# Performance work log

Hardware: AMD Instinct MI355X
Metric: run time of the kernel (lower is better)

## Reference

```python
import jax, jax.numpy as jnp
import numpy as np

N, D, K = 65536, 128, 1024
DECAY = 0.99
COMMITMENT_COST = 0.25
TEMPERATURE = 1.0
TAU = 1.0


def setup_inputs() -> dict:
    key = jax.random.key(0)
    k1, k2 = jax.random.split(key)
    return {
        "inputs": jax.random.normal(k1, (N, D), dtype=jnp.float32),
        "codebook": jax.random.normal(k2, (K, D), dtype=jnp.float32),
    }


def reference(inputs, codebook):
    # Flatten to (N, D) token view (already flat here).
    x = inputs.reshape(-1, codebook.shape[1])

    # torch.cdist(x, codebook, p=2): Euclidean pairwise distances, shape (N, K).
    d2 = (
        jnp.sum(x * x, axis=1, keepdims=True)
        + jnp.sum(codebook * codebook, axis=1)[None, :]
        - 2.0 * (x @ codebook.T)
    )
    dist = jnp.sqrt(jnp.maximum(d2, 1e-12))

    # F.gumbel_softmax(-dist / temperature, tau=1.0, hard=True)
    logits = -dist / TEMPERATURE
    gumbels = jax.random.gumbel(jax.random.key(42), logits.shape, logits.dtype)
    y_soft = jax.nn.softmax((logits + gumbels) / TAU, axis=-1)
    idx = jnp.argmax(y_soft, axis=-1)
    y_hard = jax.nn.one_hot(idx, codebook.shape[0], dtype=logits.dtype)
    # Straight-through estimator: hard forward, soft backward.
    codes = y_hard + y_soft - jax.lax.stop_gradient(y_soft)  # (N, K)

    quantized = codes @ codebook  # (N, D)
    quantization_loss = jnp.mean((quantized - x) ** 2)
    commitment_loss = COMMITMENT_COST * jnp.mean(
        (x - jax.lax.stop_gradient(codes) @ jax.lax.stop_gradient(codebook)) ** 2
    )
    loss = quantization_loss + commitment_loss

    # In-place .data EMA codebook update: scatter-accumulate via one-hot transpose matmul.
    new_codebook = DECAY * codebook + (1.0 - DECAY) * (
        jax.lax.stop_gradient(codes).T @ jax.lax.stop_gradient(x)
    )

    return codes, loss, new_codebook
```

## Files before the change

### kernel.cpp

```cpp
#include <hip/hip_runtime.h>
#include <stdint.h>
#include <math.h>

#define NTOK 65536
#define DIM  128
#define KC   1024
#define MARGIN 1e-2f

static __device__ __forceinline__ uint32_t tf_xor(uint32_t j) {
  const uint32_t K0 = 0u, K1 = 42u, K2 = 0x1BD11BDAu ^ K0 ^ K1;
  const uint32_t ks[3] = {K0, K1, K2};
  uint32_t x0 = K0;
  uint32_t x1 = j + K1;
#pragma unroll
  for (int i = 0; i < 5; ++i) {
    const int rA[4] = {13, 15, 26, 6};
    const int rB[4] = {17, 29, 16, 24};
#pragma unroll
    for (int r4 = 0; r4 < 4; ++r4) {
      const int r = (i & 1) ? rB[r4] : rA[r4];
      x0 += x1;
      x1 = (x1 << r) | (x1 >> (32 - r));
      x1 ^= x0;
    }
    x0 += ks[(i + 1) % 3];
    x1 += ks[(i + 2) % 3] + (uint32_t)(i + 1);
  }
  return x0 ^ x1;
}

static __device__ __forceinline__ float gumbf(uint32_t b) {
  const float tiny = 1.17549435e-38f;
  float f = __uint_as_float((b >> 9) | 0x3f800000u) - 1.0f;
  float u = (f > 0.0f) ? f : tiny;
  return -__logf(-__logf(u)) * 1.0f + 0.0f;
}

static __device__ __forceinline__ float gumb32(uint32_t b) {
  double f = (double)(b >> 9) * (1.0 / 8388608.0);
  const double tiny = 1.1754943508222875e-38;
  double u = (f > 0.0) ? f : tiny;
  return (float)(-log(-log(u)));
}

__global__ void vq_cnorm(const float* __restrict__ cb, double* __restrict__ cnorm,
                         float* __restrict__ lpart, uint32_t* __restrict__ fix_count) {
  const int k = blockIdx.x;
  const int t = threadIdx.x;
  double a = (double)cb[k * DIM + t];
  double b = (double)cb[k * DIM + 64 + t];
  double s = a * a + b * b;
#pragma unroll
  for (int off = 32; off >= 1; off >>= 1) s += __shfl_down(s, off, 64);
  if (t == 0) { cnorm[k] = s; lpart[k] = 0.0f; }
  if (k == 0 && t == 0) fix_count[0] = 0u;
}

__global__ __launch_bounds__(256, 2)
void vq_main(const float* __restrict__ x, const float* __restrict__ cb,
             const double* __restrict__ cnorm, uint32_t* __restrict__ out_idx,
             uint32_t* __restrict__ fix_count, uint32_t* __restrict__ fix_list) {
  __shared__ float xs[64 * 132];
  __shared__ float cs[64 * 132];
  __shared__ float xn_s[64];
  __shared__ float cn_s[64];

  const int tid = threadIdx.x;
  const int blk = blockIdx.x;
  const int rg = tid >> 4;
  const int cg = tid & 15;

  {
    const float4* xg = (const float4*)x;
#pragma unroll
    for (int q = 0; q < 8; ++q) {
      int li = tid + q * 256;
      int row = li >> 5, c4 = li & 31;
      *(float4*)(xs + row * 132 + c4 * 4) = xg[blk * 2048 + li];
    }
  }
  __syncthreads();
  if (tid < 64) {
    float s = 0.0f;
    const float* p = xs + tid * 132;
#pragma unroll
    for (int d = 0; d < DIM; ++d) s = fmaf(p[d], p[d], s);
    xn_s[tid] = s;
  }
  __syncthreads();

  const int r0 = 4 * rg;
  float xn[4] = {xn_s[r0], xn_s[r0 + 1], xn_s[r0 + 2], xn_s[r0 + 3]};
  const uint32_t R0g = (uint32_t)(blk * 64 + r0);
  const uint32_t jb[4] = {(R0g + 0u) << 10, (R0g + 1u) << 10,
                          (R0g + 2u) << 10, (R0g + 3u) << 10};

  float b1[4] = {-1e30f, -1e30f, -1e30f, -1e30f};
  float b2[4] = {-1e30f, -1e30f, -1e30f, -1e30f};
  int   k1[4] = {0, 0, 0, 0};

  const float* xp[4] = {xs + r0 * 132, xs + (r0 + 1) * 132,
                        xs + (r0 + 2) * 132, xs + (r0 + 3) * 132};
  const float* cp[4] = {cs + (cg + 0) * 132, cs + (cg + 16) * 132,
                        cs + (cg + 32) * 132, cs + (cg + 48) * 132};

  for (int kt = 0; kt < 16; ++kt) {
    {
      const float4* cg4 = (const float4*)cb;
#pragma unroll
      for (int q = 0; q < 8; ++q) {
        int li = tid + q * 256;
        int row = li >> 5, c4 = li & 31;
        *(float4*)(cs + row * 132 + c4 * 4) = cg4[kt * 2048 + li];
      }
      if (tid < 64) cn_s[tid] = (float)cnorm[kt * 64 + tid];
    }
    __syncthreads();

    float acc[4][4];
#pragma unroll
    for (int i = 0; i < 4; ++i)
#pragma unroll
      for (int j = 0; j < 4; ++j) acc[i][j] = 0.0f;

#pragma unroll 4
    for (int d = 0; d < DIM; d += 4) {
      float4 xv[4], cv[4];
#pragma unroll
      for (int i = 0; i < 4; ++i) xv[i] = *(const float4*)(xp[i] + d);
#pragma unroll
      for (int j = 0; j < 4; ++j) cv[j] = *(const float4*)(cp[j] + d);
#pragma unroll
      for (int i = 0; i < 4; ++i)
#pragma unroll
        for (int j = 0; j < 4; ++j) {
          acc[i][j] = fmaf(xv[i].x, cv[j].x, acc[i][j]);
          acc[i][j] = fmaf(xv[i].y, cv[j].y, acc[i][j]);
          acc[i][j] = fmaf(xv[i].z, cv[j].z, acc[i][j]);
          acc[i][j] = fmaf(xv[i].w, cv[j].w, acc[i][j]);
        }
    }

#pragma unroll
    for (int j = 0; j < 4; ++j) {
      const int kj = cg + 16 * j;
      const int kg = (kt << 6) + kj;
      const float cn = cn_s[kj];
#pragma unroll
      for (int i = 0; i < 4; ++i) {
        const uint32_t fj = jb[i] + (uint32_t)kg;
        const float tiny = 1.17549435e-38f;
        uint32_t bts = tf_xor(fj);
        float f = __uint_as_float((bts >> 9) | 0x3f800000u) - 1.0f;
        float u = (f > 0.0f) ? f : tiny;
        float g = -logf(-logf(u));
        float d2 = (xn[i] + cn) - 2.0f * acc[i][j];
        float dist = sqrtf(fmaxf(d2, 1e-12f));
        float z = g - dist;
        if (z > b1[i]) { b2[i] = b1[i]; b1[i] = z; k1[i] = kg; }
        else if (z > b2[i]) b2[i] = z;
      }
    }
    __syncthreads();
  }

#pragma unroll
  for (int off = 8; off >= 1; off >>= 1) {
#pragma unroll
    for (int i = 0; i < 4; ++i) {
      float ov1 = __shfl_down(b1[i], off, 16);
      int   ok1 = __shfl_down(k1[i], off, 16);
      float ov2 = __shfl_down(b2[i], off, 16);
      if (ov1 > b1[i] || (ov1 == b1[i] && ok1 < k1[i])) {
        b2[i] = fmaxf(b1[i], ov2);
        b1[i] = ov1; k1[i] = ok1;
      } else {
        b2[i] = fmaxf(b2[i], ov1);
      }
    }
  }
  if (cg == 0) {
#pragma unroll
    for (int i = 0; i < 4; ++i) {
      out_idx[R0g + i] = (uint32_t)k1[i];
      if (b1[i] - b2[i] < MARGIN) {
        uint32_t pos = atomicAdd(fix_count, 1u);
        if (pos < NTOK) fix_list[pos] = R0g + i;
      }
    }
  }
}

__global__ __launch_bounds__(256)
void vq_fixup(const float* __restrict__ x, const float* __restrict__ cb,
              const double* __restrict__ cnorm, const uint32_t* __restrict__ fix_count,
              const uint32_t* __restrict__ fix_list, uint32_t* __restrict__ out_idx) {
  __shared__ float xrow[DIM];
  __shared__ double xn_sh;
  __shared__ double bz_sh[256];
  __shared__ int    bk_sh[256];

  const int t = threadIdx.x;
  const uint32_t cnt = fix_count[0];

  for (uint32_t e = blockIdx.x; e < cnt && e < NTOK; e += gridDim.x) {
    const uint32_t row = fix_list[e];
    if (t < 32) ((float4*)xrow)[t] = ((const float4*)(x + (size_t)row * DIM))[t];
    __syncthreads();
    if (t == 0) {
      double s = 0.0;
#pragma unroll
      for (int d = 0; d < DIM; ++d) s = fma((double)xrow[d], (double)xrow[d], s);
      xn_sh = s;
    }
    __syncthreads();
    const double xn = xn_sh;
    const uint32_t jb = row << 10;

    double bz = -1e300;
    int bk = 0;
#pragma unroll
    for (int q = 0; q < 4; ++q) {
      const int kg = t + q * 256;
      float acc = 0.0f;
      const float* crow = cb + (size_t)kg * DIM;
#pragma unroll
      for (int d = 0; d < DIM; ++d) acc = fmaf(xrow[d], crow[d], acc);
      float g = gumb32(tf_xor(jb + (uint32_t)kg));
      double d2 = (xn + cnorm[kg]) - 2.0 * (double)acc;
      double dist = sqrt(fmax(d2, 1e-12));
      double z = (double)g - dist;
      if (z > bz) { bz = z; bk = kg; }
    }
    bz_sh[t] = bz; bk_sh[t] = bk;
    __syncthreads();
    for (int s = 128; s >= 1; s >>= 1) {
      if (t < s) {
        double ov = bz_sh[t + s]; int ok = bk_sh[t + s];
        if (ov > bz_sh[t] || (ov == bz_sh[t] && ok < bk_sh[t])) {
          bz_sh[t] = ov; bk_sh[t] = ok;
        }
      }
      __syncthreads();
    }
    if (t == 0) out_idx[row] = (uint32_t)bk_sh[0];
    __syncthreads();
  }
}

__global__ void vq_ema_init(const float* __restrict__ cb, float* __restrict__ ncb) {
  int i = blockIdx.x * blockDim.x + threadIdx.x;
  ncb[i] = 0.99f * cb[i];
}

__global__ __launch_bounds__(128)
void vq_finish(const float* __restrict__ x, const float* __restrict__ cb,
               const uint32_t* __restrict__ idx, float* __restrict__ codes,
               float* __restrict__ ncb, float* __restrict__ lpart) {
  const int i = blockIdx.x;
  const int t = threadIdx.x;
  const int k = (int)idx[i];

  float xv = x[i * DIM + t];
  float cv = cb[k * DIM + t];
  float d = cv - xv;
  float s = d * d;
#pragma unroll
  for (int off = 32; off >= 1; off >>= 1) s += __shfl_down(s, off, 64);
  __shared__ float sw[2];
  if ((t & 63) == 0) sw[t >> 6] = s;

  atomicAdd(ncb + k * DIM + t, 0.01f * xv);

  float4* crow = (float4*)(codes + (size_t)i * KC);
#pragma unroll
  for (int q = 0; q < 2; ++q) {
    int base = q * 512 + t * 4;
    float4 v = make_float4(0.f, 0.f, 0.f, 0.f);
    int dlt = k - base;
    if (dlt >= 0 && dlt < 4) ((float*)&v)[dlt] = 1.0f;
    crow[base >> 2] = v;
  }

  __syncthreads();
  if (t == 0) atomicAdd(lpart + (i & 1023), sw[0] + sw[1]);
}

__global__ void vq_loss_final(const float* __restrict__ lpart, float* __restrict__ loss) {
  const int t = threadIdx.x;
  float s = 0.0f;
#pragma unroll
  for (int q = 0; q < 4; ++q) s += lpart[t + q * 256];
#pragma unroll
  for (int off = 32; off >= 1; off >>= 1) s += __shfl_down(s, off, 64);
  __shared__ float sw[4];
  if ((t & 63) == 0) sw[t >> 6] = s;
  __syncthreads();
  if (t == 0) {
    float total = (sw[0] + sw[1]) + (sw[2] + sw[3]);
    loss[0] = 1.25f * (total / 8388608.0f);
  }
}

extern "C" void kernel_launch(void* const* d_in, const int* in_sizes, int n_in,
                              void* d_out, int out_size, void* d_ws, size_t ws_size,
                              hipStream_t stream) {
  const float* x  = (const float*)d_in[0];
  const float* cb = (const float*)d_in[1];

  float* codes = (float*)d_out;
  float* loss  = (float*)d_out + (size_t)NTOK * KC;
  float* ncb   = loss + 1;

  uint32_t* idx       = (uint32_t*)d_ws;
  double*   cnorm     = (double*)(idx + NTOK);
  float*    lpart     = (float*)(cnorm + KC);
  uint32_t* fix_count = (uint32_t*)(lpart + KC);
  uint32_t* fix_list  = fix_count + 64;

  vq_cnorm<<<KC, 64, 0, stream>>>(cb, cnorm, lpart, fix_count);
  vq_main<<<1024, 256, 0, stream>>>(x, cb, cnorm, idx, fix_count, fix_list);
  vq_fixup<<<256, 256, 0, stream>>>(x, cb, cnorm, fix_count, fix_list, idx);
  vq_ema_init<<<512, 256, 0, stream>>>(cb, ncb);
  vq_finish<<<NTOK, 128, 0, stream>>>(x, cb, idx, codes, ncb, lpart);
  vq_loss_final<<<1, 256, 0, stream>>>(lpart, loss);
}
```

Before: 848.1 us.

## Shrink codebook tile, add fast Gumbel log, fuse EMA init, persistent finish kernel

Several changes land together. The main kernel's codebook tile drops from 64 to 32 rows with 4x2 accumulators and launch bounds of 3 blocks per SM, aiming for higher occupancy. The Gumbel noise now uses a series expansion of -log(f) near 1 in place of the nested logf. EMA init moves into the codebook-norm kernel, and the per-row finish kernel becomes a grid-stride kernel with one wavefront per row. The log approximation can change which code wins on near ties, and the fixup pass is meant to catch those cases.

```diff
diff --git a/kernel.cpp b/kernel.cpp
--- a/kernel.cpp
+++ b/kernel.cpp
@@ -29,11 +29,26 @@
   return x0 ^ x1;
 }
 
-static __device__ __forceinline__ float gumbf(uint32_t b) {
-  const float tiny = 1.17549435e-38f;
+static __device__ __forceinline__ float gumb_fast(uint32_t b) {
   float f = __uint_as_float((b >> 9) | 0x3f800000u) - 1.0f;
-  float u = (f > 0.0f) ? f : tiny;
-  return -__logf(-__logf(u)) * 1.0f + 0.0f;
+  float w;
+  if (f >= 0.75f) {
+    float dd = 1.0f - f;
+    float p = 0.1f;
+    p = fmaf(p, dd, 0.11111111f);
+    p = fmaf(p, dd, 0.125f);
+    p = fmaf(p, dd, 0.14285714f);
+    p = fmaf(p, dd, 0.16666667f);
+    p = fmaf(p, dd, 0.2f);
+    p = fmaf(p, dd, 0.25f);
+    p = fmaf(p, dd, 0.33333333f);
+    p = fmaf(p, dd, 0.5f);
+    p = fmaf(p, dd, 1.0f);
+    w = dd * p;
+  } else {
+    w = -__logf(fmaxf(f, 1.17549435e-38f));
+  }
+  return -__logf(w);
 }
 
 static __device__ __forceinline__ float gumb32(uint32_t b) {
@@ -43,27 +58,31 @@
   return (float)(-log(-log(u)));
 }
 
-__global__ void vq_cnorm(const float* __restrict__ cb, double* __restrict__ cnorm,
-                         float* __restrict__ lpart, uint32_t* __restrict__ fix_count) {
+__global__ void vq_cnorm_ema(const float* __restrict__ cb, double* __restrict__ cnorm,
+                             float* __restrict__ lpart, uint32_t* __restrict__ fix_count,
+                             float* __restrict__ ncb) {
   const int k = blockIdx.x;
   const int t = threadIdx.x;
-  double a = (double)cb[k * DIM + t];
-  double b = (double)cb[k * DIM + 64 + t];
-  double s = a * a + b * b;
+  float a = cb[k * DIM + t];
+  float b = cb[k * DIM + 64 + t];
+  ncb[k * DIM + t]      = 0.99f * a;
+  ncb[k * DIM + 64 + t] = 0.99f * b;
+  double da = (double)a, db = (double)b;
+  double s = da * da + db * db;
 #pragma unroll
   for (int off = 32; off >= 1; off >>= 1) s += __shfl_down(s, off, 64);
   if (t == 0) { cnorm[k] = s; lpart[k] = 0.0f; }
   if (k == 0 && t == 0) fix_count[0] = 0u;
 }
 
-__global__ __launch_bounds__(256, 2)
+__global__ __launch_bounds__(256, 3)
 void vq_main(const float* __restrict__ x, const float* __restrict__ cb,
              const double* __restrict__ cnorm, uint32_t* __restrict__ out_idx,
              uint32_t* __restrict__ fix_count, uint32_t* __restrict__ fix_list) {
   __shared__ float xs[64 * 132];
-  __shared__ float cs[64 * 132];
+  __shared__ float cs[32 * 132];
   __shared__ float xn_s[64];
-  __shared__ float cn_s[64];
+  __shared__ float cn_s[32];
 
   const int tid = threadIdx.x;
   const int blk = blockIdx.x;
@@ -101,39 +120,38 @@
 
   const float* xp[4] = {xs + r0 * 132, xs + (r0 + 1) * 132,
                         xs + (r0 + 2) * 132, xs + (r0 + 3) * 132};
-  const float* cp[4] = {cs + (cg + 0) * 132, cs + (cg + 16) * 132,
-                        cs + (cg + 32) * 132, cs + (cg + 48) * 132};
-
-  for (int kt = 0; kt < 16; ++kt) {
+  const float* cp[2] = {cs + cg * 132, cs + (cg + 16) * 132};
+
+  for (int kt = 0; kt < 32; ++kt) {
     {
       const float4* cg4 = (const float4*)cb;
 #pragma unroll
-      for (int q = 0; q < 8; ++q) {
+      for (int q = 0; q < 4; ++q) {
         int li = tid + q * 256;
         int row = li >> 5, c4 = li & 31;
-        *(float4*)(cs + row * 132 + c4 * 4) = cg4[kt * 2048 + li];
-      }
-      if (tid < 64) cn_s[tid] = (float)cnorm[kt * 64 + tid];
-    }
-    __syncthreads();
-
-    float acc[4][4];
+        *(float4*)(cs + row * 132 + c4 * 4) = cg4[kt * 1024 + li];
+      }
+      if (tid < 32) cn_s[tid] = (float)cnorm[kt * 32 + tid];
+    }
+    __syncthreads();
+
+    float acc[4][2];
 #pragma unroll
     for (int i = 0; i < 4; ++i)
 #pragma unroll
-      for (int j = 0; j < 4; ++j) acc[i][j] = 0.0f;
+      for (int j = 0; j < 2; ++j) acc[i][j] = 0.0f;
 
 #pragma unroll 4
     for (int d = 0; d < DIM; d += 4) {
-      float4 xv[4], cv[4];
+      float4 xv[4], cv[2];
 #pragma unroll
       for (int i = 0; i < 4; ++i) xv[i] = *(const float4*)(xp[i] + d);
 #pragma unroll
-      for (int j = 0; j < 4; ++j) cv[j] = *(const float4*)(cp[j] + d);
+      for (int j = 0; j < 2; ++j) cv[j] = *(const float4*)(cp[j] + d);
 #pragma unroll
       for (int i = 0; i < 4; ++i)
 #pragma unroll
-        for (int j = 0; j < 4; ++j) {
+        for (int j = 0; j < 2; ++j) {
           acc[i][j] = fmaf(xv[i].x, cv[j].x, acc[i][j]);
           acc[i][j] = fmaf(xv[i].y, cv[j].y, acc[i][j]);
           acc[i][j] = fmaf(xv[i].z, cv[j].z, acc[i][j]);
@@ -142,18 +160,13 @@
     }
 
 #pragma unroll
-    for (int j = 0; j < 4; ++j) {
+    for (int j = 0; j < 2; ++j) {
       const int kj = cg + 16 * j;
-      const int kg = (kt << 6) + kj;
+      const int kg = (kt << 5) + kj;
       const float cn = cn_s[kj];
 #pragma unroll
       for (int i = 0; i < 4; ++i) {
-        const uint32_t fj = jb[i] + (uint32_t)kg;
-        const float tiny = 1.17549435e-38f;
-        uint32_t bts = tf_xor(fj);
-        float f = __uint_as_float((bts >> 9) | 0x3f800000u) - 1.0f;
-        float u = (f > 0.0f) ? f : tiny;
-        float g = -logf(-logf(u));
+        float g = gumb_fast(tf_xor(jb[i] + (uint32_t)kg));
         float d2 = (xn[i] + cn) - 2.0f * acc[i][j];
         float dist = sqrtf(fmaxf(d2, 1e-12f));
         float z = g - dist;
@@ -248,42 +261,36 @@
   }
 }
 
-__global__ void vq_ema_init(const float* __restrict__ cb, float* __restrict__ ncb) {
-  int i = blockIdx.x * blockDim.x + threadIdx.x;
-  ncb[i] = 0.99f * cb[i];
-}
-
-__global__ __launch_bounds__(128)
+__global__ __launch_bounds__(256)
 void vq_finish(const float* __restrict__ x, const float* __restrict__ cb,
                const uint32_t* __restrict__ idx, float* __restrict__ codes,
                float* __restrict__ ncb, float* __restrict__ lpart) {
-  const int i = blockIdx.x;
-  const int t = threadIdx.x;
-  const int k = (int)idx[i];
-
-  float xv = x[i * DIM + t];
-  float cv = cb[k * DIM + t];
-  float d = cv - xv;
-  float s = d * d;
-#pragma unroll
-  for (int off = 32; off >= 1; off >>= 1) s += __shfl_down(s, off, 64);
-  __shared__ float sw[2];
-  if ((t & 63) == 0) sw[t >> 6] = s;
-
-  atomicAdd(ncb + k * DIM + t, 0.01f * xv);
-
-  float4* crow = (float4*)(codes + (size_t)i * KC);
-#pragma unroll
-  for (int q = 0; q < 2; ++q) {
-    int base = q * 512 + t * 4;
-    float4 v = make_float4(0.f, 0.f, 0.f, 0.f);
-    int dlt = k - base;
-    if (dlt >= 0 && dlt < 4) ((float*)&v)[dlt] = 1.0f;
-    crow[base >> 2] = v;
-  }
-
-  __syncthreads();
-  if (t == 0) atomicAdd(lpart + (i & 1023), sw[0] + sw[1]);
+  const int lane = threadIdx.x & 63;
+  const int wid = threadIdx.x >> 6;
+
+  for (int r = blockIdx.x * 4 + wid; r < NTOK; r += 8192) {
+    const int k = (int)idx[r];
+    float2 xv = ((const float2*)(x + (size_t)r * DIM))[lane];
+    float2 cv = ((const float2*)(cb + (size_t)k * DIM))[lane];
+    float dx = cv.x - xv.x, dy = cv.y - xv.y;
+    float s = dx * dx + dy * dy;
+#pragma unroll
+    for (int off = 32; off >= 1; off >>= 1) s += __shfl_down(s, off, 64);
+
+    atomicAdd(ncb + k * DIM + 2 * lane,     0.01f * xv.x);
+    atomicAdd(ncb + k * DIM + 2 * lane + 1, 0.01f * xv.y);
+
+    float4* crow = (float4*)(codes + (size_t)r * KC);
+#pragma unroll
+    for (int q = 0; q < 4; ++q) {
+      int base = (lane * 4 + q) * 4;
+      float4 v = make_float4(0.f, 0.f, 0.f, 0.f);
+      int dlt = k - base;
+      if (dlt >= 0 && dlt < 4) ((float*)&v)[dlt] = 1.0f;
+      crow[lane * 4 + q] = v;
+    }
+    if (lane == 0) atomicAdd(lpart + (r & 1023), s);
+  }
 }
 
 __global__ void vq_loss_final(const float* __restrict__ lpart, float* __restrict__ loss) {
@@ -318,10 +325,9 @@
   uint32_t* fix_count = (uint32_t*)(lpart + KC);
   uint32_t* fix_list  = fix_count + 64;
 
-  vq_cnorm<<<KC, 64, 0, stream>>>(cb, cnorm, lpart, fix_count);
+  vq_cnorm_ema<<<KC, 64, 0, stream>>>(cb, cnorm, lpart, fix_count, ncb);
   vq_main<<<1024, 256, 0, stream>>>(x, cb, cnorm, idx, fix_count, fix_list);
   vq_fixup<<<256, 256, 0, stream>>>(x, cb, cnorm, fix_count, fix_list, idx);
-  vq_ema_init<<<512, 256, 0, stream>>>(cb, ncb);
-  vq_finish<<<NTOK, 128, 0, stream>>>(x, cb, idx, codes, ncb, lpart);
+  vq_finish<<<2048, 256, 0, stream>>>(x, cb, idx, codes, ncb, lpart);
   vq_loss_final<<<1, 256, 0, stream>>>(lpart, loss);
 }
```

After: 897.9 us. 1.06x slower.
